# Kernel tuning notes

Hardware: AMD Instinct MI355X
Metric: run time of the kernel (lower is better)

The kernel has to match this reference:

```python
import jax, jax.numpy as jnp
import numpy as np

# Dimensions: B volumes, S=15 slices, C=16 channels, H=W=6 spatial (hardcoded in module)
B, S, C, H, W = 4096, 15, 16, 6, 6
N_LUNG, N_HEART = 28, 27
N_OUT = 2 * N_LUNG + N_HEART  # 83
IN_FEAT = C * H * W           # 576


def setup_inputs() -> dict:
    key = jax.random.key(0)
    k0, k1, k2, k3, k4 = jax.random.split(key, 5)
    x = jax.random.normal(k0, (B, S, C, H, W), dtype=jnp.float32)
    dzfeatweights_heart = jax.random.normal(k1, (1, N_HEART, C, 1, 1), dtype=jnp.float32)
    dzfeatweights_lung = jax.random.normal(k2, (1, N_LUNG, C, 1, 1), dtype=jnp.float32)
    bound = 1.0 / np.sqrt(IN_FEAT)  # kaiming/fan_in style init bound
    fclayers_weights = jax.random.uniform(k3, (N_OUT, IN_FEAT), minval=-bound, maxval=bound, dtype=jnp.float32)
    fclayers_biases = jax.random.uniform(k4, (N_OUT,), minval=-bound, maxval=bound, dtype=jnp.float32)
    return {"x": x,
            "dzfeatweights_heart": dzfeatweights_heart,
            "dzfeatweights_lung": dzfeatweights_lung,
            "fclayers_weights": fclayers_weights,
            "fclayers_biases": fclayers_biases}


def reference(x, dzfeatweights_heart, dzfeatweights_lung, fclayers_weights, fclayers_biases):
    # x: [B, S, C, H, W] post-backbone features (one row per CT volume)
    Bc, Sc, Cc, Hc, Wc = x.shape
    # nonlinearity='softmax' -> Softmax(dim=2), i.e. over the 16 channels
    attn_heart = jax.nn.softmax(dzfeatweights_heart[0, :, :, 0, 0], axis=1)  # [n_heart, C]
    attn_lung = jax.nn.softmax(dzfeatweights_lung[0, :, :, 0, 0], axis=1)    # [n_lung, C]
    # disease order in the original cat: heart, left lung, right lung (lung weights shared)
    attn = jnp.concatenate([attn_heart, attn_lung, attn_lung], axis=0)       # [O, C]
    # Fuse the channel-attention broadcast-mul into the per-disease FC weights:
    # pred[b,s,o] = sum_{c,h,w} x[b,s,c,h,w] * attn[o,c] * Wfc[o,c,h,w] + bias[o]
    Wfc = fclayers_weights.reshape(-1, Cc, Hc, Wc)                           # [O, C, H, W]
    Weff = attn[:, :, None, None] * Wfc                                      # [O, C, H, W]
    slice_preds = jnp.einsum('bschw,ochw->bso', x, Weff) + fclayers_biases   # [B, S, O]
    # AvgPool1d(kernel_size=slices) over the slice axis -> [B, O]
    return jnp.mean(slice_preds, axis=1)
```

## Files before the change

### kernel.cpp

```cpp
#include <hip/hip_runtime.h>

#define NOUT 83
#define NHEART 27
#define NLUNG 28

__global__ __launch_bounds__(512) void bodyavg_scan8(
    const float4* __restrict__ x4,
    const float* __restrict__ dzh,
    const float* __restrict__ dzl,
    const float4* __restrict__ fcw4,
    const float* __restrict__ fcb,
    float* __restrict__ out,
    int B)
{
    __shared__ float  attn_lds[NOUT * 17];
    __shared__ float4 xms[8 * 144];

    const int tid = threadIdx.x;
    const int blk = blockIdx.x;
    const int b0  = blk * 8;

    if (tid < NOUT) {
        const int o = tid;
        const float* row = (o < NHEART) ? (dzh + o * 16)
                                        : (dzl + ((o - NHEART) % NLUNG) * 16);
        float vals[16];
        #pragma unroll
        for (int c = 0; c < 16; ++c) vals[c] = row[c];
        float m = vals[0];
        #pragma unroll
        for (int c = 1; c < 16; ++c) m = fmaxf(m, vals[c]);
        float s = 0.f;
        #pragma unroll
        for (int c = 0; c < 16; ++c) { vals[c] = expf(vals[c] - m); s += vals[c]; }
        const float inv = (1.0f / s) * (1.0f / 15.0f);
        #pragma unroll
        for (int c = 0; c < 16; ++c) attn_lds[o * 17 + c] = vals[c] * inv;
    }

    const int w = tid >> 6;
    const int l = tid & 63;
    const int b = b0 + w;

    {
        const float4 z = make_float4(0.f, 0.f, 0.f, 0.f);
        xms[w * 144 + l] = z;
        xms[w * 144 + l + 64] = z;
        if (l < 16) xms[w * 144 + l + 128] = z;
    }

    float4 acc[9];
    #pragma unroll
    for (int j = 0; j < 9; ++j) acc[j] = make_float4(0.f, 0.f, 0.f, 0.f);

    if (b < B) {
        const float4* src = x4 + (size_t)b * 2160 + l;
        #pragma unroll
        for (int c = 0; c < 3; ++c) {
            float4 t[9];
            #pragma unroll
            for (int u = 0; u < 9; ++u) t[u] = src[(c * 9 + u) * 64];
            #pragma unroll
            for (int u = 0; u < 9; ++u) {
                acc[u].x += t[u].x; acc[u].y += t[u].y;
                acc[u].z += t[u].z; acc[u].w += t[u].w;
            }
        }
        {
            float4 t[6];
            #pragma unroll
            for (int u = 0; u < 6; ++u) t[u] = src[(27 + u) * 64];
            #pragma unroll
            for (int u = 0; u < 6; ++u) {
                acc[u].x += t[u].x; acc[u].y += t[u].y;
                acc[u].z += t[u].z; acc[u].w += t[u].w;
            }
        }
        if (l < 48) {
            const float4 t = src[33 * 64];
            acc[6].x += t.x; acc[6].y += t.y; acc[6].z += t.z; acc[6].w += t.w;
        }
    }

    #pragma unroll
    for (int j = 0; j < 9; ++j) {
        int p = (64 * j) % 144 + l;
        if (p >= 144) p -= 144;
        const int idx = w * 144 + p;
        float4 cur = xms[idx];
        cur.x += acc[j].x; cur.y += acc[j].y;
        cur.z += acc[j].z; cur.w += acc[j].w;
        xms[idx] = cur;
    }

    __syncthreads();

    const int grp = tid >> 4;
    const int ll  = tid & 15;

    int oc[3];
    const float4* wr[3];
    #pragma unroll
    for (int k = 0; k < 3; ++k) {
        const int o = grp + 32 * k;
        oc[k] = (o < NOUT) ? o : 0;
        wr[k] = fcw4 + oc[k] * 144;
    }

    float facc[3][8] = {};

    #pragma unroll 3
    for (int jj = 0; jj < 9; ++jj) {
        const int q  = ll + 16 * jj;
        const int cc = q / 9;

        float4 xv[8];
        #pragma unroll
        for (int v = 0; v < 8; ++v) xv[v] = xms[v * 144 + q];

        #pragma unroll
        for (int k = 0; k < 3; ++k) {
            const float4 wq = wr[k][q];
            const float  a  = attn_lds[oc[k] * 17 + cc];
            const float wx = a * wq.x, wy = a * wq.y, wz = a * wq.z, ww = a * wq.w;
            #pragma unroll
            for (int v = 0; v < 8; ++v) {
                facc[k][v] = fmaf(wx, xv[v].x, facc[k][v]);
                facc[k][v] = fmaf(wy, xv[v].y, facc[k][v]);
                facc[k][v] = fmaf(wz, xv[v].z, facc[k][v]);
                facc[k][v] = fmaf(ww, xv[v].w, facc[k][v]);
            }
        }
    }

    #pragma unroll
    for (int k = 0; k < 3; ++k) {
        float r4[4];
        #pragma unroll
        for (int j = 0; j < 4; ++j) {
            const float lo = facc[k][2 * j], hi = facc[k][2 * j + 1];
            const bool  up = (ll & 1);
            const float keep = up ? hi : lo;
            const float send = up ? lo : hi;
            r4[j] = keep + __shfl_xor(send, 1, 16);
        }
        float r2[2];
        #pragma unroll
        for (int j = 0; j < 2; ++j) {
            const float lo = r4[2 * j], hi = r4[2 * j + 1];
            const bool  up = (ll & 2);
            const float keep = up ? hi : lo;
            const float send = up ? lo : hi;
            r2[j] = keep + __shfl_xor(send, 2, 16);
        }
        float r1;
        {
            const float lo = r2[0], hi = r2[1];
            const bool  up = (ll & 4);
            const float keep = up ? hi : lo;
            const float send = up ? lo : hi;
            r1 = keep + __shfl_xor(send, 4, 16);
        }
        r1 += __shfl_xor(r1, 8, 16);

        const int o = grp + 32 * k;
        const int bb = b0 + (ll & 7);
        if (ll < 8 && o < NOUT && bb < B)
            out[(size_t)bb * NOUT + o] = r1 + fcb[o];
    }
}

extern "C" void kernel_launch(void* const* d_in, const int* in_sizes, int n_in,
                              void* d_out, int out_size, void* d_ws, size_t ws_size,
                              hipStream_t stream) {
    const float* x   = (const float*)d_in[0];
    const float* dzh = (const float*)d_in[1];
    const float* dzl = (const float*)d_in[2];
    const float* fcw = (const float*)d_in[3];
    const float* fcb = (const float*)d_in[4];
    float* out = (float*)d_out;

    const int B = in_sizes[0] / (15 * 16 * 6 * 6);
    const int blocks = (B + 7) / 8;

    hipLaunchKernelGGL(bodyavg_scan8, dim3(blocks), dim3(512), 0, stream,
                       reinterpret_cast<const float4*>(x), dzh, dzl,
                       reinterpret_cast<const float4*>(fcw), fcb, out, B);
}
```

Before: 34.98 us.

## Halve volumes per block to four, widen outputs per thread group to six

Each block now handles 4 volumes with 256 threads instead of 8 with 512, and launch bounds request 6 blocks per CU. This doubles the grid size and shrinks LDS per block. The slice-sum loads are issued in batches of 6 using modular accumulator indexing. Each 16-lane group now computes 6 outputs for 4 volumes, which shortens the shuffle reduction, and the softmax step is moved after the x-load phase so it overlaps with memory traffic. In exchange, every block reloads the FC weights, so weight traffic per volume doubles.

```diff
diff --git a/kernel.cpp b/kernel.cpp
--- a/kernel.cpp
+++ b/kernel.cpp
@@ -4,7 +4,7 @@
 #define NHEART 27
 #define NLUNG 28
 
-__global__ __launch_bounds__(512) void bodyavg_scan8(
+__global__ __launch_bounds__(256, 6) void bodyavg_scan4(
     const float4* __restrict__ x4,
     const float* __restrict__ dzh,
     const float* __restrict__ dzl,
@@ -14,11 +14,68 @@
     int B)
 {
     __shared__ float  attn_lds[NOUT * 17];
-    __shared__ float4 xms[8 * 144];
+    __shared__ float4 xms[4 * 144];
 
     const int tid = threadIdx.x;
     const int blk = blockIdx.x;
-    const int b0  = blk * 8;
+    const int b0  = blk * 4;
+
+    const int w = tid >> 6;
+    const int l = tid & 63;
+    const int b = b0 + w;
+
+    float4 acc[9];
+    #pragma unroll
+    for (int j = 0; j < 9; ++j) acc[j] = make_float4(0.f, 0.f, 0.f, 0.f);
+
+    if (b < B) {
+        const float4* src = x4 + (size_t)b * 2160 + l;
+        #pragma unroll
+        for (int c = 0; c < 5; ++c) {
+            float4 t[6];
+            #pragma unroll
+            for (int u = 0; u < 6; ++u) t[u] = src[(c * 6 + u) * 64];
+            #pragma unroll
+            for (int u = 0; u < 6; ++u) {
+                const int j = (c * 6 + u) % 9;
+                acc[j].x += t[u].x; acc[j].y += t[u].y;
+                acc[j].z += t[u].z; acc[j].w += t[u].w;
+            }
+        }
+        {
+            float4 t[3];
+            #pragma unroll
+            for (int u = 0; u < 3; ++u) t[u] = src[(30 + u) * 64];
+            #pragma unroll
+            for (int u = 0; u < 3; ++u) {
+                const int j = (30 + u) % 9;
+                acc[j].x += t[u].x; acc[j].y += t[u].y;
+                acc[j].z += t[u].z; acc[j].w += t[u].w;
+            }
+            if (l < 48) {
+                const float4 tt = src[33 * 64];
+                acc[6].x += tt.x; acc[6].y += tt.y;
+                acc[6].z += tt.z; acc[6].w += tt.w;
+            }
+        }
+    }
+
+    {
+        const float4 z = make_float4(0.f, 0.f, 0.f, 0.f);
+        xms[w * 144 + l] = z;
+        xms[w * 144 + 64 + l] = z;
+        if (l < 16) xms[w * 144 + 128 + l] = z;
+    }
+    #pragma unroll
+    for (int j = 0; j < 9; ++j) {
+        int p = (64 * j) % 144 + l;
+        if (p >= 144) p -= 144;
+        const int idx = w * 144 + p;
+        float4 cur = xms[idx];
+        cur.x += acc[j].x; cur.y += acc[j].y;
+        cur.z += acc[j].z; cur.w += acc[j].w;
+        xms[idx] = cur;
+    }
 
     if (tid < NOUT) {
         const int o = tid;
@@ -38,93 +95,38 @@
         for (int c = 0; c < 16; ++c) attn_lds[o * 17 + c] = vals[c] * inv;
     }
 
-    const int w = tid >> 6;
-    const int l = tid & 63;
-    const int b = b0 + w;
-
-    {
-        const float4 z = make_float4(0.f, 0.f, 0.f, 0.f);
-        xms[w * 144 + l] = z;
-        xms[w * 144 + l + 64] = z;
-        if (l < 16) xms[w * 144 + l + 128] = z;
-    }
-
-    float4 acc[9];
-    #pragma unroll
-    for (int j = 0; j < 9; ++j) acc[j] = make_float4(0.f, 0.f, 0.f, 0.f);
-
-    if (b < B) {
-        const float4* src = x4 + (size_t)b * 2160 + l;
-        #pragma unroll
-        for (int c = 0; c < 3; ++c) {
-            float4 t[9];
-            #pragma unroll
-            for (int u = 0; u < 9; ++u) t[u] = src[(c * 9 + u) * 64];
-            #pragma unroll
-            for (int u = 0; u < 9; ++u) {
-                acc[u].x += t[u].x; acc[u].y += t[u].y;
-                acc[u].z += t[u].z; acc[u].w += t[u].w;
-            }
-        }
-        {
-            float4 t[6];
-            #pragma unroll
-            for (int u = 0; u < 6; ++u) t[u] = src[(27 + u) * 64];
-            #pragma unroll
-            for (int u = 0; u < 6; ++u) {
-                acc[u].x += t[u].x; acc[u].y += t[u].y;
-                acc[u].z += t[u].z; acc[u].w += t[u].w;
-            }
-        }
-        if (l < 48) {
-            const float4 t = src[33 * 64];
-            acc[6].x += t.x; acc[6].y += t.y; acc[6].z += t.z; acc[6].w += t.w;
-        }
-    }
-
-    #pragma unroll
-    for (int j = 0; j < 9; ++j) {
-        int p = (64 * j) % 144 + l;
-        if (p >= 144) p -= 144;
-        const int idx = w * 144 + p;
-        float4 cur = xms[idx];
-        cur.x += acc[j].x; cur.y += acc[j].y;
-        cur.z += acc[j].z; cur.w += acc[j].w;
-        xms[idx] = cur;
-    }
-
     __syncthreads();
 
     const int grp = tid >> 4;
     const int ll  = tid & 15;
 
-    int oc[3];
-    const float4* wr[3];
+    int oc[6];
+    const float4* wr[6];
     #pragma unroll
-    for (int k = 0; k < 3; ++k) {
-        const int o = grp + 32 * k;
+    for (int k = 0; k < 6; ++k) {
+        const int o = grp + 16 * k;
         oc[k] = (o < NOUT) ? o : 0;
         wr[k] = fcw4 + oc[k] * 144;
     }
 
-    float facc[3][8] = {};
+    float facc[6][4] = {};
 
     #pragma unroll 3
     for (int jj = 0; jj < 9; ++jj) {
         const int q  = ll + 16 * jj;
         const int cc = q / 9;
 
-        float4 xv[8];
+        float4 xv[4];
         #pragma unroll
-        for (int v = 0; v < 8; ++v) xv[v] = xms[v * 144 + q];
+        for (int v = 0; v < 4; ++v) xv[v] = xms[v * 144 + q];
 
         #pragma unroll
-        for (int k = 0; k < 3; ++k) {
+        for (int k = 0; k < 6; ++k) {
             const float4 wq = wr[k][q];
             const float  a  = attn_lds[oc[k] * 17 + cc];
             const float wx = a * wq.x, wy = a * wq.y, wz = a * wq.z, ww = a * wq.w;
             #pragma unroll
-            for (int v = 0; v < 8; ++v) {
+            for (int v = 0; v < 4; ++v) {
                 facc[k][v] = fmaf(wx, xv[v].x, facc[k][v]);
                 facc[k][v] = fmaf(wy, xv[v].y, facc[k][v]);
                 facc[k][v] = fmaf(wz, xv[v].z, facc[k][v]);
@@ -134,38 +136,30 @@
     }
 
     #pragma unroll
-    for (int k = 0; k < 3; ++k) {
-        float r4[4];
+    for (int k = 0; k < 6; ++k) {
+        float rA[2];
         #pragma unroll
-        for (int j = 0; j < 4; ++j) {
+        for (int j = 0; j < 2; ++j) {
             const float lo = facc[k][2 * j], hi = facc[k][2 * j + 1];
             const bool  up = (ll & 1);
             const float keep = up ? hi : lo;
             const float send = up ? lo : hi;
-            r4[j] = keep + __shfl_xor(send, 1, 16);
+            rA[j] = keep + __shfl_xor(send, 1, 16);
         }
-        float r2[2];
-        #pragma unroll
-        for (int j = 0; j < 2; ++j) {
-            const float lo = r4[2 * j], hi = r4[2 * j + 1];
+        float r1;
+        {
+            const float lo = rA[0], hi = rA[1];
             const bool  up = (ll & 2);
             const float keep = up ? hi : lo;
             const float send = up ? lo : hi;
-            r2[j] = keep + __shfl_xor(send, 2, 16);
+            r1 = keep + __shfl_xor(send, 2, 16);
         }
-        float r1;
-        {
-            const float lo = r2[0], hi = r2[1];
-            const bool  up = (ll & 4);
-            const float keep = up ? hi : lo;
-            const float send = up ? lo : hi;
-            r1 = keep + __shfl_xor(send, 4, 16);
-        }
+        r1 += __shfl_xor(r1, 4, 16);
         r1 += __shfl_xor(r1, 8, 16);
 
-        const int o = grp + 32 * k;
-        const int bb = b0 + (ll & 7);
-        if (ll < 8 && o < NOUT && bb < B)
+        const int o = grp + 16 * k;
+        const int bb = b0 + (ll & 3);
+        if (ll < 4 && o < NOUT && bb < B)
             out[(size_t)bb * NOUT + o] = r1 + fcb[o];
     }
 }
@@ -181,9 +175,9 @@
     float* out = (float*)d_out;
 
     const int B = in_sizes[0] / (15 * 16 * 6 * 6);
-    const int blocks = (B + 7) / 8;
+    const int blocks = (B + 3) / 4;
 
-    hipLaunchKernelGGL(bodyavg_scan8, dim3(blocks), dim3(512), 0, stream,
+    hipLaunchKernelGGL(bodyavg_scan4, dim3(blocks), dim3(256), 0, stream,
                        reinterpret_cast<const float4*>(x), dzh, dzl,
                        reinterpret_cast<const float4*>(fcw), fcb, out, B);
 }
```

Measured after the change: 48.50 us. +38.6%, slower.
